# Kernel optimization log

Measured on AMD Instinct MI355X. Metric: run time of the kernel, lower is better.

The kernel has to match this reference:

```python
import jax, jax.numpy as jnp
import numpy as np

B, N, D, E, FF, K = 2, 1024, 768, 8, 4, 2
H = D * FF  # 3072


def _xavier_uniform(key, shape, gain=1.0):
    # shape is (..., out, in) like torch Linear weight; fan_in/out from last two dims
    fan_out, fan_in = shape[-2], shape[-1]
    limit = gain * np.sqrt(6.0 / (fan_in + fan_out))
    return jax.random.uniform(key, shape, jnp.float32, -limit, limit)


def setup_inputs() -> dict:
    key = jax.random.key(0)
    ks = jax.random.split(key, 5)
    tokens = jax.random.normal(ks[0], (B, N, D), jnp.float32)
    # Token-choice top-K routing: softmax over experts, keep top-K weights
    logits = jax.random.normal(ks[1], (B, N, E), jnp.float32)
    probs = jax.nn.softmax(logits, axis=-1)
    topv, topi = jax.lax.top_k(probs, K)              # (B,N,K)
    onehot = jax.nn.one_hot(topi, E, dtype=jnp.float32)  # (B,N,K,E)
    combine_weights = jnp.einsum('bnk,bnke->bne', topv, onehot)  # (B,N,E)
    dispatch_weights = (combine_weights > 0).astype(jnp.float32)
    # Stacked expert weights (torch Linear convention: W is (out, in), y = x @ W.T)
    Wg = _xavier_uniform(ks[2], (E, H, D))
    Wv = _xavier_uniform(ks[3], (E, H, D))
    Wo = _xavier_uniform(ks[4], (E, D, H), gain=0.02)
    scale = jnp.full((E,), 1.0 / E, jnp.float32)  # output_scale init = 1/E
    return dict(tokens=tokens, dispatch_weights=dispatch_weights,
                combine_weights=combine_weights, Wg=Wg, Wv=Wv, Wo=Wo, scale=scale)


def reference(tokens, dispatch_weights, combine_weights, Wg, Wv, Wo, scale):
    Bb, Nn, Dd = tokens.shape
    Ee = Wg.shape[0]
    x = tokens.reshape(Bb * Nn, Dd)                    # (T, D)
    mask = (dispatch_weights.reshape(-1, Ee) > 0).astype(x.dtype)  # (T, E)
    comb = combine_weights.reshape(-1, Ee) * mask      # zero where not dispatched
    # SwiGLU-style expert FFN, all experts in one grouped contraction
    gate = jax.nn.gelu(jnp.einsum('td,ehd->teh', x, Wg), approximate=False)  # (T,E,H)
    value = jnp.einsum('td,ehd->teh', x, Wv)           # (T,E,H)
    expert_out = jnp.einsum('teh,edh->ted', gate * value, Wo) * scale[None, :, None]  # (T,E,D)
    # Weighted combine: sum_e comb[t,e] * expert_out[t,e,:]
    y = jnp.einsum('ted,te->td', expert_out, comb)     # (T, D)
    return y.reshape(Bb, Nn, Dd)
```

## Files before the change

kernel.cpp:

```cpp
#include <hip/hip_runtime.h>
#include <hip/hip_bf16.h>
#include <math.h>

#define T_TOK 2048
#define DIM   768
#define NEXP  8
#define HDIM  3072
#define MAXP  (T_TOK * 2)
#define LDST  40
#define NTILE_MAX 40

typedef __attribute__((ext_vector_type(8))) short bfrag;
typedef __attribute__((ext_vector_type(4))) float f32x4;

__device__ __forceinline__ unsigned short f2bf(float f) {
  union { float f; unsigned int u; } x; x.f = f;
  unsigned int r = x.u + 0x7fffu + ((x.u >> 16) & 1u);
  return (unsigned short)(r >> 16);
}

__global__ void k_route(const float* __restrict__ disp,
                        const float* __restrict__ comb,
                        int* __restrict__ meta,
                        float* __restrict__ row_comb,
                        int* __restrict__ row_token,
                        int* __restrict__ tok2pair) {
  __shared__ int s_cnt[NEXP], s_off[NEXP], s_cur[NEXP];
  __shared__ int s_tn[T_TOK];
  int tid = threadIdx.x;
  if (tid < NEXP) s_cnt[tid] = 0;
  for (int t = tid; t < T_TOK; t += 256) s_tn[t] = 0;
  __syncthreads();
  for (int t = tid; t < T_TOK; t += 256)
    for (int e = 0; e < NEXP; ++e)
      if (disp[t * NEXP + e] > 0.f) atomicAdd(&s_cnt[e], 1);
  __syncthreads();
  if (tid == 0) {
    int acc = 0;
    for (int e = 0; e < NEXP; ++e) { s_off[e] = acc; acc += s_cnt[e]; }
  }
  __syncthreads();
  if (tid < NEXP) {
    s_cur[tid] = s_off[tid];
    meta[tid] = s_cnt[tid];
    meta[NEXP + tid] = s_off[tid];
  }
  __syncthreads();
  for (int t = tid; t < T_TOK; t += 256)
    for (int e = 0; e < NEXP; ++e)
      if (disp[t * NEXP + e] > 0.f) {
        int p = atomicAdd(&s_cur[e], 1);
        row_token[p] = t;
        row_comb[p] = comb[t * NEXP + e];
        int sl = atomicAdd(&s_tn[t], 1);
        tok2pair[t * 2 + sl] = p;
      }
  __syncthreads();
  if (tid == 0) {
    int nt = 0;
    for (int e = 0; e < NEXP; ++e)
      for (int m0 = 0; m0 < s_cnt[e]; m0 += 128)
        meta[17 + nt++] = (e << 16) | (m0 >> 7);
    meta[16] = nt;
  }
}

__global__ void k_xbf(const float* __restrict__ X, unsigned short* __restrict__ Xb) {
  size_t i = ((size_t)blockIdx.x * 256 + threadIdx.x) * 8;
  float4 a = *(const float4*)(X + i);
  float4 b = *(const float4*)(X + i + 4);
  unsigned short r[8];
  r[0]=f2bf(a.x); r[1]=f2bf(a.y); r[2]=f2bf(a.z); r[3]=f2bf(a.w);
  r[4]=f2bf(b.x); r[5]=f2bf(b.y); r[6]=f2bf(b.z); r[7]=f2bf(b.w);
  *(uint4*)(Xb + i) = *(uint4*)r;
}

template<int WBF>
__global__ __launch_bounds__(256, 2) void k_gemm_gv_t(
    const unsigned short* __restrict__ Xb,
    const float* __restrict__ Wg,
    const float* __restrict__ Wv,
    const unsigned short* __restrict__ Wgh,
    const unsigned short* __restrict__ Wvh,
    const int* __restrict__ meta,
    const int* __restrict__ row_token,
    unsigned short* __restrict__ ubuf)
{
  int blk = blockIdx.x;
  int t = blk % NTILE_MAX;
  int nt = blk / NTILE_MAX;
  if (t >= meta[16]) return;
  int tv = meta[17 + t];
  int e = tv >> 16, m0 = (tv & 0xffff) << 7;
  int cnt = meta[e], off = meta[NEXP + e];
  int n0 = nt * 128;

  __shared__ unsigned short As[128 * LDST];
  __shared__ unsigned short Bgs[128 * LDST];
  __shared__ unsigned short Bvs[128 * LDST];

  int tid = threadIdx.x;
  int wid = tid >> 6, lane = tid & 63;
  int wm = (wid >> 1) * 64, wn = (wid & 1) * 64;
  int lr = lane & 15, quad = lane >> 4;

  int a_tok[2];
#pragma unroll
  for (int r = 0; r < 2; ++r) {
    int row = (tid + 256 * r) >> 2;
    int gr = m0 + row; if (gr >= cnt) gr = cnt - 1;
    a_tok[r] = row_token[off + gr];
  }

  const float* Wgb = Wg + (size_t)e * ((size_t)HDIM * DIM);
  const float* Wvb = Wv + (size_t)e * ((size_t)HDIM * DIM);
  const unsigned short* Wghb = Wgh + (size_t)e * ((size_t)HDIM * DIM);
  const unsigned short* Wvhb = Wvh + (size_t)e * ((size_t)HDIM * DIM);

  f32x4 zero4 = {0.f, 0.f, 0.f, 0.f};
  f32x4 accg[4][4], accv[4][4];
#pragma unroll
  for (int i = 0; i < 4; ++i)
#pragma unroll
    for (int j = 0; j < 4; ++j) { accg[i][j] = zero4; accv[i][j] = zero4; }

  for (int k0 = 0; k0 < DIM; k0 += 32) {
    __syncthreads();
#pragma unroll
    for (int r = 0; r < 2; ++r) {
      int c = tid + 256 * r;
      int row = c >> 2, sub = c & 3;
      uint4 av = *(const uint4*)(Xb + (size_t)a_tok[r] * DIM + k0 + sub * 8);
      *(uint4*)(&As[row * LDST + sub * 8]) = av;
    }
    if constexpr (WBF) {
#pragma unroll
      for (int r = 0; r < 2; ++r) {
        int c = tid + 256 * r;
        int row = c >> 2, sub = c & 3;
        uint4 gv = *(const uint4*)(Wghb + (size_t)(n0 + row) * DIM + k0 + sub * 8);
        *(uint4*)(&Bgs[row * LDST + sub * 8]) = gv;
        uint4 vv = *(const uint4*)(Wvhb + (size_t)(n0 + row) * DIM + k0 + sub * 8);
        *(uint4*)(&Bvs[row * LDST + sub * 8]) = vv;
      }
    } else {
#pragma unroll
      for (int r = 0; r < 4; ++r) {
        int c = tid + 256 * r;
        int row = c >> 3, c4 = c & 7;
        float4 gv = *(const float4*)(Wgb + (size_t)(n0 + row) * DIM + k0 + c4 * 4);
        ushort4 gp;
        gp.x = f2bf(gv.x); gp.y = f2bf(gv.y); gp.z = f2bf(gv.z); gp.w = f2bf(gv.w);
        *(ushort4*)(&Bgs[row * LDST + c4 * 4]) = gp;
        float4 vv = *(const float4*)(Wvb + (size_t)(n0 + row) * DIM + k0 + c4 * 4);
        ushort4 vp;
        vp.x = f2bf(vv.x); vp.y = f2bf(vv.y); vp.z = f2bf(vv.z); vp.w = f2bf(vv.w);
        *(ushort4*)(&Bvs[row * LDST + c4 * 4]) = vp;
      }
    }
    __syncthreads();
    bfrag a[4], bg[4], bv[4];
#pragma unroll
    for (int i = 0; i < 4; ++i)
      a[i] = *(const bfrag*)(&As[(wm + i * 16 + lr) * LDST + quad * 8]);
#pragma unroll
    for (int j = 0; j < 4; ++j) {
      bg[j] = *(const bfrag*)(&Bgs[(wn + j * 16 + lr) * LDST + quad * 8]);
      bv[j] = *(const bfrag*)(&Bvs[(wn + j * 16 + lr) * LDST + quad * 8]);
    }
#pragma unroll
    for (int i = 0; i < 4; ++i)
#pragma unroll
      for (int j = 0; j < 4; ++j) {
        accg[i][j] = __builtin_amdgcn_mfma_f32_16x16x32_bf16(a[i], bg[j], accg[i][j], 0, 0, 0);
        accv[i][j] = __builtin_amdgcn_mfma_f32_16x16x32_bf16(a[i], bv[j], accv[i][j], 0, 0, 0);
      }
  }

#pragma unroll
  for (int i = 0; i < 4; ++i)
#pragma unroll
    for (int rg = 0; rg < 4; ++rg) {
      int gr = m0 + wm + i * 16 + quad * 4 + rg;
      if (gr < cnt) {
        size_t base = (size_t)(off + gr) * HDIM + n0 + wn;
#pragma unroll
        for (int j = 0; j < 4; ++j) {
          float g = accg[i][j][rg];
          float v = accv[i][j][rg];
          float u = 0.5f * g * (1.0f + erff(g * 0.70710678118654752f)) * v;
          ubuf[base + j * 16 + lr] = f2bf(u);
        }
      }
    }
}

template<int WBF>
__global__ __launch_bounds__(256, 2) void k_gemm_out_t(
    const unsigned short* __restrict__ U,
    const float* __restrict__ Wo,
    const unsigned short* __restrict__ Woh,
    const float* __restrict__ scale,
    const int* __restrict__ meta,
    const int* __restrict__ row_token,
    const float* __restrict__ row_comb,
    float* __restrict__ partial,
    float* __restrict__ out,
    int mode)
{
  int blk = blockIdx.x;
  int t = blk % NTILE_MAX;
  int rest = blk / NTILE_MAX;
  int nt = rest % 6;
  int ks = rest / 6;
  if (t >= meta[16]) return;
  int tv = meta[17 + t];
  int e = tv >> 16, m0 = (tv & 0xffff) << 7;
  int cnt = meta[e], off = meta[NEXP + e];
  int n0 = nt * 128;
  int kbase = ks * (HDIM / 4);

  __shared__ unsigned short As[128 * LDST];
  __shared__ unsigned short Bs[128 * LDST];

  int tid = threadIdx.x;
  int wid = tid >> 6, lane = tid & 63;
  int wm = (wid >> 1) * 64, wn = (wid & 1) * 64;
  int lr = lane & 15, quad = lane >> 4;

  int a_grow[2];
#pragma unroll
  for (int r = 0; r < 2; ++r) {
    int row = (tid + 256 * r) >> 2;
    int gr = m0 + row; if (gr >= cnt) gr = cnt - 1;
    a_grow[r] = off + gr;
  }

  const float* Wb = Wo + (size_t)e * ((size_t)DIM * HDIM);
  const unsigned short* Wbh = Woh + (size_t)e * ((size_t)DIM * HDIM);

  f32x4 zero4 = {0.f, 0.f, 0.f, 0.f};
  f32x4 acc[4][4];
#pragma unroll
  for (int i = 0; i < 4; ++i)
#pragma unroll
    for (int j = 0; j < 4; ++j) acc[i][j] = zero4;

  for (int kk = 0; kk < HDIM / 4; kk += 32) {
    int k0 = kbase + kk;
    __syncthreads();
#pragma unroll
    for (int r = 0; r < 2; ++r) {
      int c = tid + 256 * r;
      int row = c >> 2, sub = c & 3;
      uint4 av = *(const uint4*)(U + (size_t)a_grow[r] * HDIM + k0 + sub * 8);
      *(uint4*)(&As[row * LDST + sub * 8]) = av;
    }
    if constexpr (WBF) {
#pragma unroll
      for (int r = 0; r < 2; ++r) {
        int c = tid + 256 * r;
        int row = c >> 2, sub = c & 3;
        uint4 bv = *(const uint4*)(Wbh + (size_t)(n0 + row) * HDIM + k0 + sub * 8);
        *(uint4*)(&Bs[row * LDST + sub * 8]) = bv;
      }
    } else {
#pragma unroll
      for (int r = 0; r < 4; ++r) {
        int c = tid + 256 * r;
        int row = c >> 3, c4 = c & 7;
        float4 bvv = *(const float4*)(Wb + (size_t)(n0 + row) * HDIM + k0 + c4 * 4);
        ushort4 bp;
        bp.x = f2bf(bvv.x); bp.y = f2bf(bvv.y); bp.z = f2bf(bvv.z); bp.w = f2bf(bvv.w);
        *(ushort4*)(&Bs[row * LDST + c4 * 4]) = bp;
      }
    }
    __syncthreads();
    bfrag a[4], b[4];
#pragma unroll
    for (int i = 0; i < 4; ++i)
      a[i] = *(const bfrag*)(&As[(wm + i * 16 + lr) * LDST + quad * 8]);
#pragma unroll
    for (int j = 0; j < 4; ++j)
      b[j] = *(const bfrag*)(&Bs[(wn + j * 16 + lr) * LDST + quad * 8]);
#pragma unroll
    for (int i = 0; i < 4; ++i)
#pragma unroll
      for (int j = 0; j < 4; ++j)
        acc[i][j] = __builtin_amdgcn_mfma_f32_16x16x32_bf16(a[i], b[j], acc[i][j], 0, 0, 0);
  }

  float sc = scale[e];
#pragma unroll
  for (int i = 0; i < 4; ++i)
#pragma unroll
    for (int rg = 0; rg < 4; ++rg) {
      int gr = m0 + wm + i * 16 + quad * 4 + rg;
      if (gr < cnt) {
        int grow = off + gr;
        float w = row_comb[grow] * sc;
        if (mode == 0) {
          float* pb = partial + ((size_t)ks * MAXP + grow) * DIM + n0 + wn;
#pragma unroll
          for (int j = 0; j < 4; ++j)
            pb[j * 16 + lr] = acc[i][j][rg] * w;
        } else {
          int tok = row_token[grow];
          float* ob = out + (size_t)tok * DIM + n0 + wn;
#pragma unroll
          for (int j = 0; j < 4; ++j)
            atomicAdd(ob + j * 16 + lr, acc[i][j][rg] * w);
        }
      }
    }
}

__global__ void k_combine(const float* __restrict__ partial,
                          const int* __restrict__ tok2pair,
                          float* __restrict__ out) {
  int idx = blockIdx.x * 256 + threadIdx.x;
  int t = idx / 192, d4 = idx % 192;
  int p0 = tok2pair[t * 2], p1 = tok2pair[t * 2 + 1];
  float sx = 0.f, sy = 0.f, sz = 0.f, sw = 0.f;
#pragma unroll
  for (int ks = 0; ks < 4; ++ks) {
    float4 a = *(const float4*)(partial + ((size_t)ks * MAXP + p0) * DIM + d4 * 4);
    float4 b = *(const float4*)(partial + ((size_t)ks * MAXP + p1) * DIM + d4 * 4);
    sx += a.x + b.x; sy += a.y + b.y; sz += a.z + b.z; sw += a.w + b.w;
  }
  float4 r; r.x = sx; r.y = sy; r.z = sz; r.w = sw;
  *(float4*)(out + (size_t)t * DIM + d4 * 4) = r;
}

extern "C" void kernel_launch(void* const* d_in, const int* in_sizes, int n_in,
                              void* d_out, int out_size, void* d_ws, size_t ws_size,
                              hipStream_t stream) {
  const float* tokens = (const float*)d_in[0];
  const float* disp   = (const float*)d_in[1];
  const float* comb   = (const float*)d_in[2];
  const float* Wg     = (const float*)d_in[3];
  const float* Wv     = (const float*)d_in[4];
  const float* Wo     = (const float*)d_in[5];
  const float* scale  = (const float*)d_in[6];
  float* out = (float*)d_out;

  char* ws = (char*)d_ws;
  int*   meta      = (int*)ws;
  int*   row_token = (int*)(ws + 16384);
  float* row_comb  = (float*)(ws + 32768);
  int*   tok2pair  = (int*)(ws + 49152);
  unsigned short* Xb   = (unsigned short*)(ws + (1ull << 20));
  unsigned short* ubuf = (unsigned short*)(ws + (5ull << 20));
  float* partial = (float*)(ws + (32ull << 20));

  const size_t need_partial = (32ull << 20) + (size_t)4 * MAXP * DIM * sizeof(float);
  const size_t need_full = 188ull << 20;
  const size_t need_mid  = 140ull << 20;

  int wbf, mode;
  unsigned short *Wgh = nullptr, *Wvh = nullptr, *Woh = nullptr;
  if (ws_size >= need_full) {
    wbf = 1; mode = 0;
    Wgh = (unsigned short*)(ws + (80ull  << 20));
    Wvh = (unsigned short*)(ws + (116ull << 20));
    Woh = (unsigned short*)(ws + (152ull << 20));
  } else if (ws_size >= need_mid) {
    wbf = 1; mode = 1;
    Wgh = (unsigned short*)(ws + (32ull  << 20));
    Wvh = (unsigned short*)(ws + (68ull  << 20));
    Woh = (unsigned short*)(ws + (104ull << 20));
  } else {
    wbf = 0;
    mode = (ws_size >= need_partial) ? 0 : 1;
  }

  hipLaunchKernelGGL(k_route, dim3(1), dim3(256), 0, stream,
                     disp, comb, meta, row_comb, row_token, tok2pair);
  hipLaunchKernelGGL(k_xbf, dim3((T_TOK * DIM) / (256 * 8)), dim3(256), 0, stream,
                     tokens, Xb);
  if (wbf) {
    const int wgrid = (NEXP * HDIM * DIM) / (256 * 8);
    hipLaunchKernelGGL(k_xbf, dim3(wgrid), dim3(256), 0, stream, Wg, Wgh);
    hipLaunchKernelGGL(k_xbf, dim3(wgrid), dim3(256), 0, stream, Wv, Wvh);
    hipLaunchKernelGGL(k_xbf, dim3(wgrid), dim3(256), 0, stream, Wo, Woh);
  }

  if (wbf)
    hipLaunchKernelGGL(HIP_KERNEL_NAME(k_gemm_gv_t<1>), dim3(NTILE_MAX * 24), dim3(256), 0, stream,
                       Xb, Wg, Wv, Wgh, Wvh, meta, row_token, ubuf);
  else
    hipLaunchKernelGGL(HIP_KERNEL_NAME(k_gemm_gv_t<0>), dim3(NTILE_MAX * 24), dim3(256), 0, stream,
                       Xb, Wg, Wv, Wgh, Wvh, meta, row_token, ubuf);

  if (mode == 1)
    hipMemsetAsync(d_out, 0, (size_t)out_size * sizeof(float), stream);

  if (wbf)
    hipLaunchKernelGGL(HIP_KERNEL_NAME(k_gemm_out_t<1>), dim3(NTILE_MAX * 6 * 4), dim3(256), 0, stream,
                       ubuf, Wo, Woh, scale, meta, row_token, row_comb, partial, out, mode);
  else
    hipLaunchKernelGGL(HIP_KERNEL_NAME(k_gemm_out_t<0>), dim3(NTILE_MAX * 6 * 4), dim3(256), 0, stream,
                       ubuf, Wo, Woh, scale, meta, row_token, row_comb, partial, out, mode);

  if (mode == 0)
    hipLaunchKernelGGL(k_combine, dim3((T_TOK * DIM / 4) / 256), dim3(256), 0, stream,
                       partial, tok2pair, out);
}
```

Before: 432.9 us.

## Fuse routing and bf16 conversions into one prep kernel; remap GEMM block order

Merges the routing kernel and the four fp32-to-bf16 conversion launches into a single kernel, where block 0 does routing and the other blocks convert tokens and weights. This removes several launches and lets routing overlap with conversion. It also remaps block indices in both GEMMs so that groups of 8 consecutive blocks share a tile and differ in N-tile, which on the 8-XCD layout may improve per-XCD cache reuse of the activation rows. Routing now runs on a single block that the conversion blocks do not wait for.

```diff
diff --git a/kernel.cpp b/kernel.cpp
--- a/kernel.cpp
+++ b/kernel.cpp
@@ -19,60 +19,80 @@
   return (unsigned short)(r >> 16);
 }
 
-__global__ void k_route(const float* __restrict__ disp,
-                        const float* __restrict__ comb,
-                        int* __restrict__ meta,
-                        float* __restrict__ row_comb,
-                        int* __restrict__ row_token,
-                        int* __restrict__ tok2pair) {
+__global__ void k_prep(const float* __restrict__ disp,
+                       const float* __restrict__ comb,
+                       int* __restrict__ meta,
+                       float* __restrict__ row_comb,
+                       int* __restrict__ row_token,
+                       int* __restrict__ tok2pair,
+                       const float* __restrict__ X, unsigned short* __restrict__ Xb,
+                       const float* __restrict__ Wg, const float* __restrict__ Wv,
+                       const float* __restrict__ Wo,
+                       unsigned short* __restrict__ Wgh, unsigned short* __restrict__ Wvh,
+                       unsigned short* __restrict__ Woh) {
   __shared__ int s_cnt[NEXP], s_off[NEXP], s_cur[NEXP];
   __shared__ int s_tn[T_TOK];
+  int b = blockIdx.x;
   int tid = threadIdx.x;
-  if (tid < NEXP) s_cnt[tid] = 0;
-  for (int t = tid; t < T_TOK; t += 256) s_tn[t] = 0;
-  __syncthreads();
-  for (int t = tid; t < T_TOK; t += 256)
-    for (int e = 0; e < NEXP; ++e)
-      if (disp[t * NEXP + e] > 0.f) atomicAdd(&s_cnt[e], 1);
-  __syncthreads();
-  if (tid == 0) {
-    int acc = 0;
-    for (int e = 0; e < NEXP; ++e) { s_off[e] = acc; acc += s_cnt[e]; }
-  }
-  __syncthreads();
-  if (tid < NEXP) {
-    s_cur[tid] = s_off[tid];
-    meta[tid] = s_cnt[tid];
-    meta[NEXP + tid] = s_off[tid];
-  }
-  __syncthreads();
-  for (int t = tid; t < T_TOK; t += 256)
-    for (int e = 0; e < NEXP; ++e)
-      if (disp[t * NEXP + e] > 0.f) {
-        int p = atomicAdd(&s_cur[e], 1);
-        row_token[p] = t;
-        row_comb[p] = comb[t * NEXP + e];
-        int sl = atomicAdd(&s_tn[t], 1);
-        tok2pair[t * 2 + sl] = p;
-      }
-  __syncthreads();
-  if (tid == 0) {
-    int nt = 0;
-    for (int e = 0; e < NEXP; ++e)
-      for (int m0 = 0; m0 < s_cnt[e]; m0 += 128)
-        meta[17 + nt++] = (e << 16) | (m0 >> 7);
-    meta[16] = nt;
-  }
-}
-
-__global__ void k_xbf(const float* __restrict__ X, unsigned short* __restrict__ Xb) {
-  size_t i = ((size_t)blockIdx.x * 256 + threadIdx.x) * 8;
-  float4 a = *(const float4*)(X + i);
-  float4 b = *(const float4*)(X + i + 4);
+  if (b == 0) {
+    if (tid < NEXP) s_cnt[tid] = 0;
+    for (int t = tid; t < T_TOK; t += 256) s_tn[t] = 0;
+    __syncthreads();
+    for (int t = tid; t < T_TOK; t += 256)
+      for (int e = 0; e < NEXP; ++e)
+        if (disp[t * NEXP + e] > 0.f) atomicAdd(&s_cnt[e], 1);
+    __syncthreads();
+    if (tid == 0) {
+      int acc = 0;
+      for (int e = 0; e < NEXP; ++e) { s_off[e] = acc; acc += s_cnt[e]; }
+    }
+    __syncthreads();
+    if (tid < NEXP) {
+      s_cur[tid] = s_off[tid];
+      meta[tid] = s_cnt[tid];
+      meta[NEXP + tid] = s_off[tid];
+    }
+    __syncthreads();
+    for (int t = tid; t < T_TOK; t += 256)
+      for (int e = 0; e < NEXP; ++e)
+        if (disp[t * NEXP + e] > 0.f) {
+          int p = atomicAdd(&s_cur[e], 1);
+          row_token[p] = t;
+          row_comb[p] = comb[t * NEXP + e];
+          int sl = atomicAdd(&s_tn[t], 1);
+          tok2pair[t * 2 + sl] = p;
+        }
+    __syncthreads();
+    if (tid == 0) {
+      int nt = 0;
+      for (int e = 0; e < NEXP; ++e)
+        for (int m0 = 0; m0 < s_cnt[e]; m0 += 128)
+          meta[17 + nt++] = (e << 16) | (m0 >> 7);
+      meta[16] = nt;
+    }
+    return;
+  }
+  int idx = b - 1;
+  const float* src;
+  unsigned short* dst;
+  size_t base;
+  if (idx < 768) {
+    src = X; dst = Xb; base = (size_t)idx * 2048;
+  } else {
+    idx -= 768;
+    int w = idx / 9216;
+    int off = idx % 9216;
+    base = (size_t)off * 2048;
+    src = (w == 0) ? Wg : (w == 1) ? Wv : Wo;
+    dst = (w == 0) ? Wgh : (w == 1) ? Wvh : Woh;
+  }
+  size_t i = base + (size_t)tid * 8;
+  float4 a = *(const float4*)(src + i);
+  float4 bb = *(const float4*)(src + i + 4);
   unsigned short r[8];
   r[0]=f2bf(a.x); r[1]=f2bf(a.y); r[2]=f2bf(a.z); r[3]=f2bf(a.w);
-  r[4]=f2bf(b.x); r[5]=f2bf(b.y); r[6]=f2bf(b.z); r[7]=f2bf(b.w);
-  *(uint4*)(Xb + i) = *(uint4*)r;
+  r[4]=f2bf(bb.x); r[5]=f2bf(bb.y); r[6]=f2bf(bb.z); r[7]=f2bf(bb.w);
+  *(uint4*)(dst + i) = *(uint4*)r;
 }
 
 template<int WBF>
@@ -87,8 +107,9 @@
     unsigned short* __restrict__ ubuf)
 {
   int blk = blockIdx.x;
-  int t = blk % NTILE_MAX;
-  int nt = blk / NTILE_MAX;
+  int xc = blk & 7, slot = blk >> 3;
+  int nt = xc + 8 * (slot / NTILE_MAX);
+  int t  = slot % NTILE_MAX;
   if (t >= meta[16]) return;
   int tv = meta[17 + t];
   int e = tv >> 16, m0 = (tv & 0xffff) << 7;
@@ -128,16 +149,16 @@
     __syncthreads();
 #pragma unroll
     for (int r = 0; r < 2; ++r) {
-      int c = tid + 256 * r;
-      int row = c >> 2, sub = c & 3;
+      int c2 = tid + 256 * r;
+      int row = c2 >> 2, sub = c2 & 3;
       uint4 av = *(const uint4*)(Xb + (size_t)a_tok[r] * DIM + k0 + sub * 8);
       *(uint4*)(&As[row * LDST + sub * 8]) = av;
     }
     if constexpr (WBF) {
 #pragma unroll
       for (int r = 0; r < 2; ++r) {
-        int c = tid + 256 * r;
-        int row = c >> 2, sub = c & 3;
+        int c2 = tid + 256 * r;
+        int row = c2 >> 2, sub = c2 & 3;
         uint4 gv = *(const uint4*)(Wghb + (size_t)(n0 + row) * DIM + k0 + sub * 8);
         *(uint4*)(&Bgs[row * LDST + sub * 8]) = gv;
         uint4 vv = *(const uint4*)(Wvhb + (size_t)(n0 + row) * DIM + k0 + sub * 8);
@@ -146,8 +167,8 @@
     } else {
 #pragma unroll
       for (int r = 0; r < 4; ++r) {
-        int c = tid + 256 * r;
-        int row = c >> 3, c4 = c & 7;
+        int c2 = tid + 256 * r;
+        int row = c2 >> 3, c4 = c2 & 7;
         float4 gv = *(const float4*)(Wgb + (size_t)(n0 + row) * DIM + k0 + c4 * 4);
         ushort4 gp;
         gp.x = f2bf(gv.x); gp.y = f2bf(gv.y); gp.z = f2bf(gv.z); gp.w = f2bf(gv.w);
@@ -209,10 +230,10 @@
     int mode)
 {
   int blk = blockIdx.x;
-  int t = blk % NTILE_MAX;
-  int rest = blk / NTILE_MAX;
-  int nt = rest % 6;
-  int ks = rest / 6;
+  int xc = blk & 7, slot = blk >> 3;
+  int sidx = xc + 8 * (slot / NTILE_MAX);
+  int nt = sidx % 6, ks = sidx / 6;
+  int t = slot % NTILE_MAX;
   if (t >= meta[16]) return;
   int tv = meta[17 + t];
   int e = tv >> 16, m0 = (tv & 0xffff) << 7;
@@ -251,24 +272,24 @@
     __syncthreads();
 #pragma unroll
     for (int r = 0; r < 2; ++r) {
-      int c = tid + 256 * r;
-      int row = c >> 2, sub = c & 3;
+      int c2 = tid + 256 * r;
+      int row = c2 >> 2, sub = c2 & 3;
       uint4 av = *(const uint4*)(U + (size_t)a_grow[r] * HDIM + k0 + sub * 8);
       *(uint4*)(&As[row * LDST + sub * 8]) = av;
     }
     if constexpr (WBF) {
 #pragma unroll
       for (int r = 0; r < 2; ++r) {
-        int c = tid + 256 * r;
-        int row = c >> 2, sub = c & 3;
+        int c2 = tid + 256 * r;
+        int row = c2 >> 2, sub = c2 & 3;
         uint4 bv = *(const uint4*)(Wbh + (size_t)(n0 + row) * HDIM + k0 + sub * 8);
         *(uint4*)(&Bs[row * LDST + sub * 8]) = bv;
       }
     } else {
 #pragma unroll
       for (int r = 0; r < 4; ++r) {
-        int c = tid + 256 * r;
-        int row = c >> 3, c4 = c & 7;
+        int c2 = tid + 256 * r;
+        int row = c2 >> 3, c4 = c2 & 7;
         float4 bvv = *(const float4*)(Wb + (size_t)(n0 + row) * HDIM + k0 + c4 * 4);
         ushort4 bp;
         bp.x = f2bf(bvv.x); bp.y = f2bf(bvv.y); bp.z = f2bf(bvv.z); bp.w = f2bf(bvv.w);
@@ -372,18 +393,13 @@
   } else {
     wbf = 0;
     mode = (ws_size >= need_partial) ? 0 : 1;
-  }
-
-  hipLaunchKernelGGL(k_route, dim3(1), dim3(256), 0, stream,
-                     disp, comb, meta, row_comb, row_token, tok2pair);
-  hipLaunchKernelGGL(k_xbf, dim3((T_TOK * DIM) / (256 * 8)), dim3(256), 0, stream,
-                     tokens, Xb);
-  if (wbf) {
-    const int wgrid = (NEXP * HDIM * DIM) / (256 * 8);
-    hipLaunchKernelGGL(k_xbf, dim3(wgrid), dim3(256), 0, stream, Wg, Wgh);
-    hipLaunchKernelGGL(k_xbf, dim3(wgrid), dim3(256), 0, stream, Wv, Wvh);
-    hipLaunchKernelGGL(k_xbf, dim3(wgrid), dim3(256), 0, stream, Wo, Woh);
-  }
+    Wgh = Wvh = Woh = (unsigned short*)Xb;
+  }
+
+  int prep_grid = wbf ? (1 + 768 + 3 * 9216) : (1 + 768);
+  hipLaunchKernelGGL(k_prep, dim3(prep_grid), dim3(256), 0, stream,
+                     disp, comb, meta, row_comb, row_token, tok2pair,
+                     tokens, Xb, Wg, Wv, Wo, Wgh, Wvh, Woh);
 
   if (wbf)
     hipLaunchKernelGGL(HIP_KERNEL_NAME(k_gemm_gv_t<1>), dim3(NTILE_MAX * 24), dim3(256), 0, stream,
```

Measured after the change: 402.8 us. 7.0% less time.
